# Kernel optimization log

Measured on AMD Instinct MI355X. Metric: run time of the kernel, lower is better.

Reference implementation:

```python
import jax, jax.numpy as jnp
import numpy as np

K = 16          # knn_graph k
FPS_RATIO = 0.5 # fps ratio
BN_EPS = 1e-5


def knn_idx(p, k):
    # p: [B, N, 3] -> neighbor indices [B, N, k] (loop=True: self included)
    n2 = jnp.sum(p * p, axis=-1)                                  # [B, N]
    d = n2[:, :, None] + n2[:, None, :] - 2.0 * jnp.einsum('bnc,bmc->bnm', p, p)
    _, idx = jax.lax.top_k(-d, k)                                 # smallest distances
    return idx


def gather_nbrs(x, idx):
    # x: [B, N, C], idx: [B, N, k] -> [B, N, k, C]
    return jax.vmap(lambda xb, ib: xb[ib])(x, idx)


def bn_silu(y, g, be):
    # training-mode BatchNorm over all rows (flattened) + SiLU, per PyG MLP defaults
    C = y.shape[-1]
    yf = y.reshape(-1, C)
    mu = jnp.mean(yf, axis=0)
    var = jnp.mean((yf - mu) ** 2, axis=0)
    return jax.nn.silu((y - mu) * jax.lax.rsqrt(var + BN_EPS) * g + be)


def fps_idx(p, m):
    # farthest point sampling on one cloud p: [N, 3], deterministic start at 0
    d0 = jnp.sum((p - p[0]) ** 2, axis=-1)
    def step(mind, _):
        i = jnp.argmax(mind)
        di = jnp.sum((p - p[i]) ** 2, axis=-1)
        return jnp.minimum(mind, di), i.astype(jnp.int32)
    _, idxs = jax.lax.scan(step, d0, None, length=m - 1)
    return jnp.concatenate([jnp.zeros((1,), jnp.int32), idxs])


def setup_inputs() -> dict:
    key = jax.random.key(0)
    ks = jax.random.split(key, 4)
    B, N, zdim = 16, 2048, 256
    return {
        'pos': jax.random.normal(ks[0], (B, N, 3), jnp.float32),
        'W1': jax.random.normal(ks[1], (6, 64), jnp.float32) * (1.0 / np.sqrt(6)),
        'b1': jnp.zeros((64,), jnp.float32),
        'g1': jnp.ones((64,), jnp.float32),
        'be1': jnp.zeros((64,), jnp.float32),
        'W2a': jax.random.normal(ks[2], (67, 128), jnp.float32) * (1.0 / np.sqrt(67)),
        'b2a': jnp.zeros((128,), jnp.float32),
        'g2a': jnp.ones((128,), jnp.float32),
        'be2a': jnp.zeros((128,), jnp.float32),
        'W2b': jax.random.normal(ks[3], (128, zdim), jnp.float32) * (1.0 / np.sqrt(128)),
        'b2b': jnp.zeros((zdim,), jnp.float32),
        'g2b': jnp.ones((zdim,), jnp.float32),
        'be2b': jnp.zeros((zdim,), jnp.float32),
    }


def reference(pos, W1, b1, g1, be1, W2a, b2a, g2a, be2a, W2b, b2b, g2b, be2b):
    B, N, _ = pos.shape
    M = int(N * FPS_RATIO)

    # conv1: knn graph on pos, message = MLP([x_j, pos_j - pos_i]), max-aggr
    idx1 = knn_idx(pos, K)                                  # [B, N, K]
    pos_j = gather_nbrs(pos, idx1)                          # [B, N, K, 3]
    msg = jnp.concatenate([pos_j, pos_j - pos[:, :, None, :]], axis=-1)  # [B,N,K,6]
    h = bn_silu(msg @ W1 + b1, g1, be1)                     # [B, N, K, 64]
    h = jnp.max(h, axis=2)                                  # [B, N, 64]

    # farthest point sampling, ratio 0.5
    idx_f = jax.vmap(fps_idx, in_axes=(0, None))(pos, M)    # [B, M]
    h = jax.vmap(lambda a, i: a[i])(h, idx_f)               # [B, M, 64]
    pos2 = jax.vmap(lambda a, i: a[i])(pos, idx_f)          # [B, M, 3]

    # conv2: knn on sampled points, message = MLP2([h_j, pos_j - pos_i]), max-aggr
    idx2 = knn_idx(pos2, K)                                 # [B, M, K]
    h_j = gather_nbrs(h, idx2)                              # [B, M, K, 64]
    p_j = gather_nbrs(pos2, idx2)                           # [B, M, K, 3]
    msg2 = jnp.concatenate([h_j, p_j - pos2[:, :, None, :]], axis=-1)  # [B,M,K,67]
    h2 = bn_silu(msg2 @ W2a + b2a, g2a, be2a)               # [B, M, K, 128]
    h2 = bn_silu(h2 @ W2b + b2b, g2b, be2b)                 # [B, M, K, zdim]
    h2 = jnp.max(h2, axis=2)                                # [B, M, zdim]

    # global max aggregation per cloud
    return jnp.max(h2, axis=1)                              # [B, zdim]
```

## Files before the change

kernel.cpp:

```cpp
#include <hip/hip_runtime.h>
#include <hip/hip_bf16.h>

#define NB 16
#define NN 2048
#define KNNK 16
#define MM 1024
#define RC1 (NB*NN*KNNK)
#define RC2 (NB*MM*KNNK)

typedef unsigned long long u64;
typedef __attribute__((ext_vector_type(8))) short short8;
typedef __attribute__((ext_vector_type(4))) float f32x4;

__device__ __forceinline__ float frn_mul(float a, float b){ return __fmul_rn(a,b); }
__device__ __forceinline__ float frn_add(float a, float b){ return __fadd_rn(a,b); }
__device__ __forceinline__ float frn_sub(float a, float b){ return __fsub_rn(a,b); }
__device__ __forceinline__ float silu_f(float x){ return x / (1.0f + __expf(-x)); }
__device__ __forceinline__ u64 umax64(u64 a, u64 b){ return a > b ? a : b; }

__device__ __forceinline__ unsigned f32_sortable(float f){
  unsigned u = __float_as_uint(f);
  return u ^ ((unsigned)((int)u >> 31) | 0x80000000u);
}
__device__ __forceinline__ unsigned short f2bf(float f){
  unsigned u = __float_as_uint(f);
  return (unsigned short)((u + 0x7FFFu + ((u >> 16) & 1u)) >> 16);
}
__device__ __forceinline__ float bf2f(unsigned short h){
  return __uint_as_float(((unsigned)h) << 16);
}

__device__ __forceinline__ void atomicMaxF(unsigned* addr, float v){
  if (v >= 0.f) atomicMax((int*)addr, (int)__float_as_uint(v));
  else          atomicMin(addr, __float_as_uint(v));
}
__device__ __forceinline__ void atomicMinF(unsigned* addr, float v){
  if (v >= 0.f) atomicMin((int*)addr, (int)__float_as_uint(v));
  else          atomicMax(addr, __float_as_uint(v));
}

__global__ __launch_bounds__(256) void init_kernel(float* stats1, float* stats2a, float* stats2b,
                                                   unsigned* gmax, unsigned* gmin){
  int t = blockIdx.x*256 + threadIdx.x;
  if (t < 128) stats1[t] = 0.f;
  if (t < 256) stats2a[t] = 0.f;
  if (t < 512) stats2b[t] = 0.f;
  if (t < 4096){ gmax[t] = 0xFF800000u; gmin[t] = 0x7F800000u; }
}

template<int CNT>
__device__ __forceinline__ void knn_scan(const float4* pts, int jbase,
                                         float xi, float yi, float zi, float n2i, u64* best){
#pragma unroll
  for (int p = 0; p < KNNK; ++p) best[p] = ~0ull;
  for (int jj = 0; jj < CNT; ++jj){
    float4 v = pts[jbase + jj];
    float e = frn_add(frn_add(frn_mul(xi,v.x), frn_mul(yi,v.y)), frn_mul(zi,v.z));
    float d = frn_sub(frn_add(n2i, v.w), frn_mul(2.0f, e));
    u64 key = ((u64)f32_sortable(d) << 32) | (unsigned)(jbase + jj);
    if (key < best[KNNK-1]){
      u64 cur = key;
#pragma unroll
      for (int p = 0; p < KNNK; ++p){
        u64 mn = best[p] < cur ? best[p] : cur;
        u64 mx = best[p] < cur ? cur : best[p];
        best[p] = mn; cur = mx;
      }
    }
  }
}

__global__ __launch_bounds__(256) void k0_fps_knn1(const float* __restrict__ pos,
    int* __restrict__ idxf, float* __restrict__ pos2, int* __restrict__ idx1,
    const float* __restrict__ W1, const float* __restrict__ b1, float* __restrict__ stats1){
  __shared__ __align__(16) char smem[77*1024];
  int tid = threadIdx.x;
  if (blockIdx.x < 16){
    int b = blockIdx.x;
    float4* pts4 = (float4*)smem;
    int* sel = (int*)(smem + 32*1024);
    u64* wred = (u64*)(smem + 36*1024);
    const float* pb = pos + (size_t)b*NN*3;
    float X[8], Y[8], Z[8], MD[8];
    unsigned LO[8];
#pragma unroll
    for (int q = 0; q < 8; ++q){
      int p = tid + 256*q;
      float x = pb[p*3+0], y = pb[p*3+1], z = pb[p*3+2];
      X[q] = x; Y[q] = y; Z[q] = z;
      LO[q] = ~(unsigned)p;
      pts4[p] = make_float4(x, y, z, 0.f);
    }
    float qx = pb[0], qy = pb[1], qz = pb[2];
#pragma unroll
    for (int q = 0; q < 8; ++q){
      float dx = frn_sub(X[q],qx), dy = frn_sub(Y[q],qy), dz = frn_sub(Z[q],qz);
      MD[q] = frn_add(frn_add(frn_mul(dx,dx), frn_mul(dy,dy)), frn_mul(dz,dz));
    }
    if (tid == 0) sel[0] = 0;
    int wv = tid >> 6;
    __syncthreads();
    for (int s = 1; s < MM; ++s){
      u64 t0 = umax64(((u64)__float_as_uint(MD[0])<<32)|LO[0], ((u64)__float_as_uint(MD[1])<<32)|LO[1]);
      u64 t1 = umax64(((u64)__float_as_uint(MD[2])<<32)|LO[2], ((u64)__float_as_uint(MD[3])<<32)|LO[3]);
      u64 t2 = umax64(((u64)__float_as_uint(MD[4])<<32)|LO[4], ((u64)__float_as_uint(MD[5])<<32)|LO[5]);
      u64 t3 = umax64(((u64)__float_as_uint(MD[6])<<32)|LO[6], ((u64)__float_as_uint(MD[7])<<32)|LO[7]);
      u64 kk = umax64(umax64(t0, t1), umax64(t2, t3));
#define RED_DPP(CTRL) { \
      unsigned lo_ = (unsigned)kk, hi_ = (unsigned)(kk>>32); \
      unsigned plo = (unsigned)__builtin_amdgcn_update_dpp((int)lo_,(int)lo_,CTRL,0xF,0xF,false); \
      unsigned phi = (unsigned)__builtin_amdgcn_update_dpp((int)hi_,(int)hi_,CTRL,0xF,0xF,false); \
      u64 o = ((u64)phi<<32)|plo; kk = o > kk ? o : kk; }
      RED_DPP(0xB1)
      RED_DPP(0x4E)
      RED_DPP(0x124)
      RED_DPP(0x128)
      RED_DPP(0x142)
      RED_DPP(0x143)
#undef RED_DPP
      int par = s & 1;
      if ((tid & 63) == 63) wred[par*4 + wv] = kk;
      __syncthreads();
      const u64* wr = wred + par*4;
      u64 K = umax64(umax64(wr[0], wr[1]), umax64(wr[2], wr[3]));
      unsigned wp = ~(unsigned)K;
      if (tid == 0) sel[s] = (int)wp;
      float4 wc = pts4[wp];
#pragma unroll
      for (int q = 0; q < 8; ++q){
        float dx = frn_sub(X[q],wc.x), dy = frn_sub(Y[q],wc.y), dz = frn_sub(Z[q],wc.z);
        float d = frn_add(frn_add(frn_mul(dx,dx), frn_mul(dy,dy)), frn_mul(dz,dz));
        MD[q] = fminf(MD[q], d);
      }
    }
    __syncthreads();
    for (int m = tid; m < MM; m += 256){
      int j = sel[m];
      idxf[b*MM + m] = j;
      float4 c = pts4[j];
      pos2[(size_t)(b*MM+m)*3+0] = c.x;
      pos2[(size_t)(b*MM+m)*3+1] = c.y;
      pos2[(size_t)(b*MM+m)*3+2] = c.z;
    }
  } else {
    int cid = blockIdx.x - 16;
    int b = cid >> 4;
    int rb16 = cid & 15;
    float4* pts4 = (float4*)smem;
    u64* cres = (u64*)(smem + 32*1024);
    int* idxl = (int*)(smem + 32*1024 + 34816);
    float* red = (float*)(smem + 32*1024 + 34816 + 8704);
    const float* pb = pos + (size_t)b*NN*3;
    for (int i = tid; i < NN; i += 256){
      float x = pb[i*3+0], y = pb[i*3+1], z = pb[i*3+2];
      float n2 = frn_add(frn_add(frn_mul(x,x), frn_mul(y,y)), frn_mul(z,z));
      pts4[i] = make_float4(x, y, z, n2);
    }
    __syncthreads();
    int lrow = tid & 127;
    int ch = tid >> 7;
    int i = rb16*128 + lrow;
    float4 qv = pts4[i];
    u64 best[KNNK];
    knn_scan<1024>(pts4, ch*1024, qv.x, qv.y, qv.z, qv.w, best);
#pragma unroll
    for (int p = 0; p < KNNK; ++p) cres[tid*17 + p] = best[p];
    __syncthreads();
    if (tid < 128){
      const u64* A = cres + tid*17;
      const u64* B = cres + (tid + 128)*17;
      int ia = 0, ib = 0;
      int* op = idx1 + ((size_t)(b*NN + rb16*128 + tid))*KNNK;
#pragma unroll
      for (int p = 0; p < KNNK; ++p){
        u64 ka = A[ia], kb = B[ib];
        int v;
        if (ka < kb){ v = (int)(unsigned)ka; ++ia; }
        else        { v = (int)(unsigned)kb; ++ib; }
        op[p] = v;
        idxl[tid*17 + p] = v;
      }
    }
    __syncthreads();
    int lane = tid & 63, wv = tid >> 6;
    float w[6];
#pragma unroll
    for (int f = 0; f < 6; ++f) w[f] = W1[f*64 + lane];
    float bias = b1[lane];
    float ssum = 0.f, ssq = 0.f;
    for (int r = 0; r < 32; ++r){
      int lr = wv*32 + r;
      float4 pi = pts4[rb16*128 + lr];
      const int* ip = idxl + lr*17;
#pragma unroll 4
      for (int k = 0; k < KNNK; ++k){
        int j = ip[k];
        float4 pj = pts4[j];
        float y = bias;
        y = fmaf(pj.x, w[0], y); y = fmaf(pj.y, w[1], y); y = fmaf(pj.z, w[2], y);
        y = fmaf(pj.x - pi.x, w[3], y); y = fmaf(pj.y - pi.y, w[4], y); y = fmaf(pj.z - pi.z, w[5], y);
        ssum += y; ssq = fmaf(y, y, ssq);
      }
    }
    red[(wv*64+lane)*2+0] = ssum; red[(wv*64+lane)*2+1] = ssq;
    __syncthreads();
    if (tid < 64){
      float s = red[(0*64+lane)*2]+red[(1*64+lane)*2]+red[(2*64+lane)*2]+red[(3*64+lane)*2];
      float q = red[(0*64+lane)*2+1]+red[(1*64+lane)*2+1]+red[(2*64+lane)*2+1]+red[(3*64+lane)*2+1];
      atomicAdd(&stats1[lane], s);
      atomicAdd(&stats1[64+lane], q);
    }
  }
}

__global__ __launch_bounds__(256) void k1_knn2_c1apply(
    const float* __restrict__ pos2, int* __restrict__ idx2,
    const float* __restrict__ pos, const int* __restrict__ idx1,
    const float* __restrict__ W1, const float* __restrict__ b1,
    const float* __restrict__ g1, const float* __restrict__ be1,
    const float* __restrict__ stats1, unsigned short* __restrict__ hbf){
  __shared__ __align__(16) char smem[48*1024];
  int tid = threadIdx.x;
  if (blockIdx.x < 256){
    int b = blockIdx.x >> 4;
    int rb = blockIdx.x & 15;
    float4* sm = (float4*)smem;
    u64* cres = (u64*)(smem + 16*1024);
    const float* pb = pos2 + (size_t)b*MM*3;
    for (int t = tid; t < MM; t += 256){
      float x = pb[t*3+0], y = pb[t*3+1], z = pb[t*3+2];
      float n2 = frn_add(frn_add(frn_mul(x,x), frn_mul(y,y)), frn_mul(z,z));
      sm[t] = make_float4(x, y, z, n2);
    }
    __syncthreads();
    int trow = tid & 63, ch = tid >> 6;
    int i = rb*64 + trow;
    float4 qv = sm[i];
    u64 best[KNNK];
    knn_scan<256>(sm, ch*256, qv.x, qv.y, qv.z, qv.w, best);
#pragma unroll
    for (int p = 0; p < KNNK; ++p) cres[tid*KNNK + p] = best[p];
    __syncthreads();
    if (tid < 64){
      const u64* L0 = cres + tid*KNNK;
      const u64* L1 = cres + (64 + tid)*KNNK;
      const u64* L2 = cres + (128 + tid)*KNNK;
      const u64* L3 = cres + (192 + tid)*KNNK;
      int o0=0, o1=0, o2=0, o3=0;
      int* op = idx2 + ((size_t)(b*MM + rb*64 + tid))*KNNK;
#pragma unroll
      for (int p = 0; p < KNNK; ++p){
        u64 k0 = L0[o0], k1 = L1[o1], k2 = L2[o2], k3 = L3[o3];
        u64 m01 = k0 < k1 ? k0 : k1;
        u64 m23 = k2 < k3 ? k2 : k3;
        u64 m = m01 < m23 ? m01 : m23;
        op[p] = (int)(unsigned)m;
        o0 += (m == k0); o1 += (m == k1); o2 += (m == k2); o3 += (m == k3);
      }
    }
  } else {
    float4* pts4 = (float4*)smem;
    int bblk = blockIdx.x - 256;
    int b = bblk >> 6;
    const float* pb = pos + (size_t)b*NN*3;
    for (int i = tid; i < NN; i += 256)
      pts4[i] = make_float4(pb[i*3+0], pb[i*3+1], pb[i*3+2], 0.f);
    __syncthreads();
    int lane = tid & 63, wv = tid >> 6;
    int wave = bblk*4 + wv;
    float w[6];
#pragma unroll
    for (int f = 0; f < 6; ++f) w[f] = W1[f*64 + lane];
    float bias = b1[lane];
    const float inv = 1.0f / (float)RC1;
    float mu = stats1[lane] * inv;
    float var = fmaxf(stats1[64+lane]*inv - mu*mu, 0.f);
    float sc = rsqrtf(var + 1e-5f) * g1[lane];
    float sh = be1[lane] - mu*sc;
    for (int r = 0; r < 8; ++r){
      int row = wave*8 + r;
      int ii = row & 2047;
      float4 pi = pts4[ii];
      const int* ip = idx1 + (size_t)row * KNNK;
      float ymn = INFINITY, ymx = -INFINITY;
#pragma unroll 4
      for (int k = 0; k < KNNK; ++k){
        int j = ip[k];
        float4 pj = pts4[j];
        float y = bias;
        y = fmaf(pj.x, w[0], y); y = fmaf(pj.y, w[1], y); y = fmaf(pj.z, w[2], y);
        y = fmaf(pj.x - pi.x, w[3], y); y = fmaf(pj.y - pi.y, w[4], y); y = fmaf(pj.z - pi.z, w[5], y);
        ymn = fminf(ymn, y); ymx = fmaxf(ymx, y);
      }
      hbf[((size_t)row << 6) + lane] = f2bf(fmaxf(silu_f(fmaf(ymx, sc, sh)), silu_f(fmaf(ymn, sc, sh))));
    }
  }
}

__global__ __launch_bounds__(256) void conv2a_kernel(
    const unsigned short* __restrict__ hbf, const int* __restrict__ idxf,
    const float* __restrict__ pos2, const int* __restrict__ idx2,
    const float* __restrict__ W2a, const float* __restrict__ b2a,
    float* __restrict__ stats2a, __hip_bfloat16* __restrict__ y2a){
  __shared__ __align__(16) unsigned short At[64*104];
  __shared__ __align__(16) unsigned short Wt[128*104];
  __shared__ int qs[64];
  int tid = threadIdx.x;
  int lane = tid & 63, wvi = tid >> 6;
  for (int i = tid; i < 96*128; i += 256){
    int k = i >> 7, c = i & 127;
    Wt[c*104 + k] = (k < 67) ? f2bf(W2a[k*128 + c]) : (unsigned short)0;
  }
  for (int i = tid; i < 64*104/2; i += 256) ((unsigned*)At)[i] = 0u;
  __syncthreads();
  int cb = wvi*32;
  short8 bfrag[2][3];
#pragma unroll
  for (int cf = 0; cf < 2; ++cf)
#pragma unroll
    for (int kf = 0; kf < 3; ++kf){
      int col = cb + cf*16 + (lane & 15);
      bfrag[cf][kf] = *(short8*)(Wt + col*104 + kf*32 + (lane>>4)*8);
    }
  float bb[2] = { b2a[cb + (lane & 15)], b2a[cb + 16 + (lane & 15)] };
  float ssum[2] = {0.f, 0.f}, ssq[2] = {0.f, 0.f};
  for (int t = 0; t < 4; ++t){
    int tbase = (blockIdx.x*4 + t)*64;
    if (t > 0) __syncthreads();
    if (tid < 64){
      int grow = tbase + tid;
      int b = grow >> 14;
      int m = (grow >> 4) & 1023;
      int j = idx2[grow];
      int q = idxf[b*MM + j];
      qs[tid] = b*NN + q;
      const float* pm = pos2 + ((size_t)(b*MM + m))*3;
      const float* pj = pos2 + ((size_t)(b*MM + j))*3;
      At[tid*104 + 64] = f2bf(pj[0]-pm[0]);
      At[tid*104 + 65] = f2bf(pj[1]-pm[1]);
      At[tid*104 + 66] = f2bf(pj[2]-pm[2]);
    }
    __syncthreads();
    {
      int r = tid & 63, ck = tid >> 6;
      const unsigned short* src = hbf + (size_t)qs[r]*64 + ck*16;
      short8 v0 = *(const short8*)(src);
      short8 v1 = *(const short8*)(src + 8);
      *(short8*)(At + r*104 + ck*16) = v0;
      *(short8*)(At + r*104 + ck*16 + 8) = v1;
    }
    __syncthreads();
#pragma unroll
    for (int rf = 0; rf < 4; ++rf){
      int r = rf*16 + (lane & 15);
      short8 af[3];
#pragma unroll
      for (int kf = 0; kf < 3; ++kf)
        af[kf] = *(short8*)(At + r*104 + kf*32 + (lane>>4)*8);
#pragma unroll
      for (int cf = 0; cf < 2; ++cf){
        f32x4 acc = {0.f,0.f,0.f,0.f};
#pragma unroll
        for (int kf = 0; kf < 3; ++kf)
          acc = __builtin_amdgcn_mfma_f32_16x16x32_bf16(af[kf], bfrag[cf][kf], acc, 0, 0, 0);
#pragma unroll
        for (int jj = 0; jj < 4; ++jj){
          int row = tbase + rf*16 + (lane>>4)*4 + jj;
          int col = cb + cf*16 + (lane & 15);
          float y = acc[jj] + bb[cf];
          ssum[cf] += y; ssq[cf] = fmaf(y, y, ssq[cf]);
          y2a[(size_t)row*128 + col] = __float2bfloat16(y);
        }
      }
    }
  }
#pragma unroll
  for (int cf = 0; cf < 2; ++cf){
#pragma unroll
    for (int off = 16; off <= 32; off += 16){
      ssum[cf] += __shfl_xor(ssum[cf], off);
      ssq[cf]  += __shfl_xor(ssq[cf],  off);
    }
  }
  if ((lane >> 4) == 0){
    atomicAdd(&stats2a[cb + lane], ssum[0]);
    atomicAdd(&stats2a[128 + cb + lane], ssq[0]);
    atomicAdd(&stats2a[cb + 16 + lane], ssum[1]);
    atomicAdd(&stats2a[128 + cb + 16 + lane], ssq[1]);
  }
}

__global__ __launch_bounds__(256) void conv2b_kernel(
    const __hip_bfloat16* __restrict__ y2a, const float* __restrict__ stats2a,
    const float* __restrict__ g2a, const float* __restrict__ be2a,
    const float* __restrict__ W2b, const float* __restrict__ b2b,
    float* __restrict__ stats2b, unsigned* __restrict__ gmax, unsigned* __restrict__ gmin){
  __shared__ __align__(16) char Albs[64*256];
  __shared__ __align__(16) char Btbs[128*256];
  __shared__ float sc2a[128], sh2a[128];
  int tid = threadIdx.x;
  int lane = tid & 63, wvi = tid >> 6;
  int ct = blockIdx.x & 1;
  int rb = blockIdx.x >> 1;
  int c0 = ct * 128;
  int batch = rb >> 5;
  if (tid < 128){
    const float inv = 1.0f / (float)RC2;
    float mu = stats2a[tid] * inv;
    float var = fmaxf(stats2a[128+tid]*inv - mu*mu, 0.f);
    float s = rsqrtf(var + 1e-5f) * g2a[tid];
    sc2a[tid] = s; sh2a[tid] = be2a[tid] - mu*s;
  }
  {
    int cc = tid & 127, u0 = tid >> 7;
#pragma unroll
    for (int i = 0; i < 8; ++i){
      int u = u0 + i*2;
      unsigned short hb[8];
#pragma unroll
      for (int e = 0; e < 8; ++e) hb[e] = f2bf(W2b[(size_t)(u*8+e)*256 + c0 + cc]);
      *(short8*)(Btbs + cc*256 + u*16) = *(short8*)hb;
    }
  }
  __syncthreads();
  short8 bfrag[2][4];
#pragma unroll
  for (int cf = 0; cf < 2; ++cf)
#pragma unroll
    for (int kb4 = 0; kb4 < 4; ++kb4){
      int col_local = wvi*32 + cf*16 + (lane & 15);
      bfrag[cf][kb4] = *(short8*)(Btbs + col_local*256 + kb4*64 + (lane>>4)*16);
    }
  float bb[2] = { b2b[c0 + wvi*32 + (lane & 15)], b2b[c0 + wvi*32 + 16 + (lane & 15)] };
  float vmn[2] = {INFINITY, INFINITY}, vmx[2] = {-INFINITY, -INFINITY};
  float ssum[2] = {0.f, 0.f}, ssq[2] = {0.f, 0.f};
  const unsigned short* y2u = (const unsigned short*)y2a;
  int sr = tid & 63, su = tid >> 6;
  for (int tile = 0; tile < 8; ++tile){
    int row0 = rb*512 + tile*64;
    if (tile > 0) __syncthreads();
#pragma unroll
    for (int i = 0; i < 4; ++i){
      int u = su + i*4;
      short8 v = *(const short8*)(y2u + (size_t)(row0 + sr)*128 + u*8);
      unsigned short ha[8];
#pragma unroll
      for (int e = 0; e < 8; ++e){
        int k = u*8 + e;
        float f = bf2f((unsigned short)v[e]);
        ha[e] = f2bf(silu_f(fmaf(f, sc2a[k], sh2a[k])));
      }
      *(short8*)(Albs + sr*256 + ((u*16) ^ ((sr & 7) << 4))) = *(short8*)ha;
    }
    __syncthreads();
#pragma unroll
    for (int sl = 0; sl < 4; ++sl){
      int r = sl*16 + (lane & 15);
      short8 af[4];
#pragma unroll
      for (int kb4 = 0; kb4 < 4; ++kb4)
        af[kb4] = *(short8*)(Albs + r*256 + ((kb4*64 + (lane>>4)*16) ^ ((r & 7) << 4)));
#pragma unroll
      for (int cf = 0; cf < 2; ++cf){
        f32x4 acc = {0.f, 0.f, 0.f, 0.f};
#pragma unroll
        for (int kb4 = 0; kb4 < 4; ++kb4)
          acc = __builtin_amdgcn_mfma_f32_16x16x32_bf16(af[kb4], bfrag[cf][kb4], acc, 0, 0, 0);
#pragma unroll
        for (int j = 0; j < 4; ++j){
          float y = acc[j] + bb[cf];
          vmn[cf] = fminf(vmn[cf], y); vmx[cf] = fmaxf(vmx[cf], y);
          ssum[cf] += y; ssq[cf] = fmaf(y, y, ssq[cf]);
        }
      }
    }
  }
#pragma unroll
  for (int cf = 0; cf < 2; ++cf){
#pragma unroll
    for (int off = 16; off <= 32; off += 16){
      vmn[cf]  = fminf(vmn[cf],  __shfl_xor(vmn[cf],  off));
      vmx[cf]  = fmaxf(vmx[cf],  __shfl_xor(vmx[cf],  off));
      ssum[cf] = ssum[cf] + __shfl_xor(ssum[cf], off);
      ssq[cf]  = ssq[cf]  + __shfl_xor(ssq[cf],  off);
    }
  }
  if ((lane >> 4) == 0){
#pragma unroll
    for (int cf = 0; cf < 2; ++cf){
      int c = c0 + wvi*32 + cf*16 + lane;
      atomicAdd(&stats2b[c], ssum[cf]);
      atomicAdd(&stats2b[256+c], ssq[cf]);
      atomicMaxF(&gmax[batch*256 + c], vmx[cf]);
      atomicMinF(&gmin[batch*256 + c], vmn[cf]);
    }
  }
}

__global__ __launch_bounds__(256) void final_kernel(
    const float* __restrict__ stats2b, const unsigned* __restrict__ gmax,
    const unsigned* __restrict__ gmin, const float* __restrict__ g2b,
    const float* __restrict__ be2b, float* __restrict__ out){
  int t = blockIdx.x*256 + threadIdx.x;
  if (t >= NB*256) return;
  int c = t & 255;
  const float inv = 1.0f / (float)RC2;
  float mu = stats2b[c]*inv;
  float var = fmaxf(stats2b[256+c]*inv - mu*mu, 0.f);
  float sc = rsqrtf(var + 1e-5f)*g2b[c];
  float sh = be2b[c] - mu*sc;
  float mx = __uint_as_float(gmax[t]);
  float mn = __uint_as_float(gmin[t]);
  out[t] = fmaxf(silu_f(fmaf(mx, sc, sh)), silu_f(fmaf(mn, sc, sh)));
}

extern "C" void kernel_launch(void* const* d_in, const int* in_sizes, int n_in,
                              void* d_out, int out_size, void* d_ws, size_t ws_size,
                              hipStream_t stream){
  (void)in_sizes; (void)n_in; (void)out_size; (void)ws_size;
  const float* pos  = (const float*)d_in[0];
  const float* W1   = (const float*)d_in[1];
  const float* b1   = (const float*)d_in[2];
  const float* g1   = (const float*)d_in[3];
  const float* be1  = (const float*)d_in[4];
  const float* W2a  = (const float*)d_in[5];
  const float* b2a  = (const float*)d_in[6];
  const float* g2a  = (const float*)d_in[7];
  const float* be2a = (const float*)d_in[8];
  const float* W2b  = (const float*)d_in[9];
  const float* b2b  = (const float*)d_in[10];
  const float* g2b  = (const float*)d_in[11];
  const float* be2b = (const float*)d_in[12];

  char* w = (char*)d_ws;
  size_t off = 0;
  auto carve = [&](size_t bytes)->void*{ void* p = w + off; off += (bytes + 255) & ~(size_t)255; return p; };
  int*      idx1    = (int*)carve((size_t)NB*NN*KNNK*4);
  unsigned short* hbf = (unsigned short*)carve((size_t)NB*NN*64*2);
  int*      idxf    = (int*)carve((size_t)NB*MM*4);
  float*    pos2    = (float*)carve((size_t)NB*MM*3*4);
  int*      idx2    = (int*)carve((size_t)NB*MM*KNNK*4);
  float*    stats1  = (float*)carve(128*4);
  float*    stats2a = (float*)carve(256*4);
  float*    stats2b = (float*)carve(512*4);
  unsigned* gmax    = (unsigned*)carve(4096*4);
  unsigned* gmin    = (unsigned*)carve(4096*4);
  __hip_bfloat16* y2a = (__hip_bfloat16*)carve((size_t)RC2*128*2);

  init_kernel<<<dim3(16), dim3(256), 0, stream>>>(stats1, stats2a, stats2b, gmax, gmin);
  k0_fps_knn1<<<dim3(272), dim3(256), 0, stream>>>(pos, idxf, pos2, idx1, W1, b1, stats1);
  k1_knn2_c1apply<<<dim3(1280), dim3(256), 0, stream>>>(pos2, idx2, pos, idx1, W1, b1, g1, be1, stats1, hbf);
  conv2a_kernel<<<dim3(1024), dim3(256), 0, stream>>>(hbf, idxf, pos2, idx2, W2a, b2a, stats2a, y2a);
  conv2b_kernel<<<dim3(1024), dim3(256), 0, stream>>>(y2a, stats2a, g2a, be2a, W2b, b2b, stats2b, gmax, gmin);
  final_kernel<<<dim3(16), dim3(256), 0, stream>>>(stats2b, gmax, gmin, g2b, be2b, (float*)d_out);
}
```

Before: 801.8 us.

## Split FPS across two kernels to overlap with knn1 and conv1 apply

Farthest point sampling is split at step 512. The first half runs alongside the knn1/stats blocks and saves its running min-distance state to global memory. The second half resumes inside the conv1-apply kernel, so the serial FPS chain overlaps with more parallel work. knn2 moves into its own kernel launched afterwards, which adds one launch and a small state round-trip through memory.

```diff
diff --git a/kernel.cpp b/kernel.cpp
--- a/kernel.cpp
+++ b/kernel.cpp
@@ -5,6 +5,7 @@
 #define NN 2048
 #define KNNK 16
 #define MM 1024
+#define FSPLIT 512
 #define RC1 (NB*NN*KNNK)
 #define RC2 (NB*MM*KNNK)
 
@@ -70,9 +71,48 @@
   }
 }
 
-__global__ __launch_bounds__(256) void k0_fps_knn1(const float* __restrict__ pos,
+__device__ __forceinline__ void fps_span(float4* pts4, int* sel, u64* wred,
+    float X[8], float Y[8], float Z[8], float MD[8], const unsigned LO[8],
+    int s0, int s1, int tid, int wv){
+  for (int s = s0; s < s1; ++s){
+    u64 t0 = umax64(((u64)__float_as_uint(MD[0])<<32)|LO[0], ((u64)__float_as_uint(MD[1])<<32)|LO[1]);
+    u64 t1 = umax64(((u64)__float_as_uint(MD[2])<<32)|LO[2], ((u64)__float_as_uint(MD[3])<<32)|LO[3]);
+    u64 t2 = umax64(((u64)__float_as_uint(MD[4])<<32)|LO[4], ((u64)__float_as_uint(MD[5])<<32)|LO[5]);
+    u64 t3 = umax64(((u64)__float_as_uint(MD[6])<<32)|LO[6], ((u64)__float_as_uint(MD[7])<<32)|LO[7]);
+    u64 kk = umax64(umax64(t0, t1), umax64(t2, t3));
+#define RED_DPP(CTRL) { \
+    unsigned lo_ = (unsigned)kk, hi_ = (unsigned)(kk>>32); \
+    unsigned plo = (unsigned)__builtin_amdgcn_update_dpp((int)lo_,(int)lo_,CTRL,0xF,0xF,false); \
+    unsigned phi = (unsigned)__builtin_amdgcn_update_dpp((int)hi_,(int)hi_,CTRL,0xF,0xF,false); \
+    u64 o = ((u64)phi<<32)|plo; kk = o > kk ? o : kk; }
+    RED_DPP(0xB1)
+    RED_DPP(0x4E)
+    RED_DPP(0x124)
+    RED_DPP(0x128)
+    RED_DPP(0x142)
+    RED_DPP(0x143)
+#undef RED_DPP
+    int par = s & 1;
+    if ((tid & 63) == 63) wred[par*4 + wv] = kk;
+    __syncthreads();
+    const u64* wr = wred + par*4;
+    u64 K = umax64(umax64(wr[0], wr[1]), umax64(wr[2], wr[3]));
+    unsigned wp = ~(unsigned)K;
+    if (tid == 0) sel[s] = (int)wp;
+    float4 wc = pts4[wp];
+#pragma unroll
+    for (int q = 0; q < 8; ++q){
+      float dx = frn_sub(X[q],wc.x), dy = frn_sub(Y[q],wc.y), dz = frn_sub(Z[q],wc.z);
+      float d = frn_add(frn_add(frn_mul(dx,dx), frn_mul(dy,dy)), frn_mul(dz,dz));
+      MD[q] = fminf(MD[q], d);
+    }
+  }
+}
+
+__global__ __launch_bounds__(256) void kA(const float* __restrict__ pos,
     int* __restrict__ idxf, float* __restrict__ pos2, int* __restrict__ idx1,
-    const float* __restrict__ W1, const float* __restrict__ b1, float* __restrict__ stats1){
+    const float* __restrict__ W1, const float* __restrict__ b1, float* __restrict__ stats1,
+    float* __restrict__ mdsave){
   __shared__ __align__(16) char smem[77*1024];
   int tid = threadIdx.x;
   if (blockIdx.x < 16){
@@ -100,41 +140,9 @@
     if (tid == 0) sel[0] = 0;
     int wv = tid >> 6;
     __syncthreads();
-    for (int s = 1; s < MM; ++s){
-      u64 t0 = umax64(((u64)__float_as_uint(MD[0])<<32)|LO[0], ((u64)__float_as_uint(MD[1])<<32)|LO[1]);
-      u64 t1 = umax64(((u64)__float_as_uint(MD[2])<<32)|LO[2], ((u64)__float_as_uint(MD[3])<<32)|LO[3]);
-      u64 t2 = umax64(((u64)__float_as_uint(MD[4])<<32)|LO[4], ((u64)__float_as_uint(MD[5])<<32)|LO[5]);
-      u64 t3 = umax64(((u64)__float_as_uint(MD[6])<<32)|LO[6], ((u64)__float_as_uint(MD[7])<<32)|LO[7]);
-      u64 kk = umax64(umax64(t0, t1), umax64(t2, t3));
-#define RED_DPP(CTRL) { \
-      unsigned lo_ = (unsigned)kk, hi_ = (unsigned)(kk>>32); \
-      unsigned plo = (unsigned)__builtin_amdgcn_update_dpp((int)lo_,(int)lo_,CTRL,0xF,0xF,false); \
-      unsigned phi = (unsigned)__builtin_amdgcn_update_dpp((int)hi_,(int)hi_,CTRL,0xF,0xF,false); \
-      u64 o = ((u64)phi<<32)|plo; kk = o > kk ? o : kk; }
-      RED_DPP(0xB1)
-      RED_DPP(0x4E)
-      RED_DPP(0x124)
-      RED_DPP(0x128)
-      RED_DPP(0x142)
-      RED_DPP(0x143)
-#undef RED_DPP
-      int par = s & 1;
-      if ((tid & 63) == 63) wred[par*4 + wv] = kk;
-      __syncthreads();
-      const u64* wr = wred + par*4;
-      u64 K = umax64(umax64(wr[0], wr[1]), umax64(wr[2], wr[3]));
-      unsigned wp = ~(unsigned)K;
-      if (tid == 0) sel[s] = (int)wp;
-      float4 wc = pts4[wp];
-#pragma unroll
-      for (int q = 0; q < 8; ++q){
-        float dx = frn_sub(X[q],wc.x), dy = frn_sub(Y[q],wc.y), dz = frn_sub(Z[q],wc.z);
-        float d = frn_add(frn_add(frn_mul(dx,dx), frn_mul(dy,dy)), frn_mul(dz,dz));
-        MD[q] = fminf(MD[q], d);
-      }
-    }
-    __syncthreads();
-    for (int m = tid; m < MM; m += 256){
+    fps_span(pts4, sel, wred, X, Y, Z, MD, LO, 1, FSPLIT, tid, wv);
+    __syncthreads();
+    for (int m = tid; m < FSPLIT; m += 256){
       int j = sel[m];
       idxf[b*MM + m] = j;
       float4 c = pts4[j];
@@ -142,6 +150,8 @@
       pos2[(size_t)(b*MM+m)*3+1] = c.y;
       pos2[(size_t)(b*MM+m)*3+2] = c.z;
     }
+#pragma unroll
+    for (int q = 0; q < 8; ++q) mdsave[b*NN + tid + 256*q] = MD[q];
   } else {
     int cid = blockIdx.x - 16;
     int b = cid >> 4;
@@ -213,54 +223,46 @@
   }
 }
 
-__global__ __launch_bounds__(256) void k1_knn2_c1apply(
-    const float* __restrict__ pos2, int* __restrict__ idx2,
-    const float* __restrict__ pos, const int* __restrict__ idx1,
+__global__ __launch_bounds__(256) void kB(const float* __restrict__ pos,
+    int* __restrict__ idxf, float* __restrict__ pos2, const int* __restrict__ idx1,
     const float* __restrict__ W1, const float* __restrict__ b1,
     const float* __restrict__ g1, const float* __restrict__ be1,
-    const float* __restrict__ stats1, unsigned short* __restrict__ hbf){
-  __shared__ __align__(16) char smem[48*1024];
+    const float* __restrict__ stats1, unsigned short* __restrict__ hbf,
+    const float* __restrict__ mdsave){
+  __shared__ __align__(16) char smem[41*1024];
   int tid = threadIdx.x;
-  if (blockIdx.x < 256){
-    int b = blockIdx.x >> 4;
-    int rb = blockIdx.x & 15;
-    float4* sm = (float4*)smem;
-    u64* cres = (u64*)(smem + 16*1024);
-    const float* pb = pos2 + (size_t)b*MM*3;
-    for (int t = tid; t < MM; t += 256){
-      float x = pb[t*3+0], y = pb[t*3+1], z = pb[t*3+2];
-      float n2 = frn_add(frn_add(frn_mul(x,x), frn_mul(y,y)), frn_mul(z,z));
-      sm[t] = make_float4(x, y, z, n2);
-    }
-    __syncthreads();
-    int trow = tid & 63, ch = tid >> 6;
-    int i = rb*64 + trow;
-    float4 qv = sm[i];
-    u64 best[KNNK];
-    knn_scan<256>(sm, ch*256, qv.x, qv.y, qv.z, qv.w, best);
-#pragma unroll
-    for (int p = 0; p < KNNK; ++p) cres[tid*KNNK + p] = best[p];
-    __syncthreads();
-    if (tid < 64){
-      const u64* L0 = cres + tid*KNNK;
-      const u64* L1 = cres + (64 + tid)*KNNK;
-      const u64* L2 = cres + (128 + tid)*KNNK;
-      const u64* L3 = cres + (192 + tid)*KNNK;
-      int o0=0, o1=0, o2=0, o3=0;
-      int* op = idx2 + ((size_t)(b*MM + rb*64 + tid))*KNNK;
-#pragma unroll
-      for (int p = 0; p < KNNK; ++p){
-        u64 k0 = L0[o0], k1 = L1[o1], k2 = L2[o2], k3 = L3[o3];
-        u64 m01 = k0 < k1 ? k0 : k1;
-        u64 m23 = k2 < k3 ? k2 : k3;
-        u64 m = m01 < m23 ? m01 : m23;
-        op[p] = (int)(unsigned)m;
-        o0 += (m == k0); o1 += (m == k1); o2 += (m == k2); o3 += (m == k3);
-      }
+  if (blockIdx.x < 16){
+    int b = blockIdx.x;
+    float4* pts4 = (float4*)smem;
+    int* sel = (int*)(smem + 32*1024);
+    u64* wred = (u64*)(smem + 36*1024);
+    const float* pb = pos + (size_t)b*NN*3;
+    float X[8], Y[8], Z[8], MD[8];
+    unsigned LO[8];
+#pragma unroll
+    for (int q = 0; q < 8; ++q){
+      int p = tid + 256*q;
+      float x = pb[p*3+0], y = pb[p*3+1], z = pb[p*3+2];
+      X[q] = x; Y[q] = y; Z[q] = z;
+      LO[q] = ~(unsigned)p;
+      pts4[p] = make_float4(x, y, z, 0.f);
+      MD[q] = mdsave[b*NN + p];
+    }
+    int wv = tid >> 6;
+    __syncthreads();
+    fps_span(pts4, sel, wred, X, Y, Z, MD, LO, FSPLIT, MM, tid, wv);
+    __syncthreads();
+    for (int m = FSPLIT + tid; m < MM; m += 256){
+      int j = sel[m];
+      idxf[b*MM + m] = j;
+      float4 c = pts4[j];
+      pos2[(size_t)(b*MM+m)*3+0] = c.x;
+      pos2[(size_t)(b*MM+m)*3+1] = c.y;
+      pos2[(size_t)(b*MM+m)*3+2] = c.z;
     }
   } else {
     float4* pts4 = (float4*)smem;
-    int bblk = blockIdx.x - 256;
+    int bblk = blockIdx.x - 16;
     int b = bblk >> 6;
     const float* pb = pos + (size_t)b*NN*3;
     for (int i = tid; i < NN; i += 256)
@@ -297,6 +299,48 @@
   }
 }
 
+__global__ __launch_bounds__(256) void k1_knn2(
+    const float* __restrict__ pos2, int* __restrict__ idx2){
+  __shared__ __align__(16) char smem[48*1024];
+  int tid = threadIdx.x;
+  int b = blockIdx.x >> 4;
+  int rb = blockIdx.x & 15;
+  float4* sm = (float4*)smem;
+  u64* cres = (u64*)(smem + 16*1024);
+  const float* pb = pos2 + (size_t)b*MM*3;
+  for (int t = tid; t < MM; t += 256){
+    float x = pb[t*3+0], y = pb[t*3+1], z = pb[t*3+2];
+    float n2 = frn_add(frn_add(frn_mul(x,x), frn_mul(y,y)), frn_mul(z,z));
+    sm[t] = make_float4(x, y, z, n2);
+  }
+  __syncthreads();
+  int trow = tid & 63, ch = tid >> 6;
+  int i = rb*64 + trow;
+  float4 qv = sm[i];
+  u64 best[KNNK];
+  knn_scan<256>(sm, ch*256, qv.x, qv.y, qv.z, qv.w, best);
+#pragma unroll
+  for (int p = 0; p < KNNK; ++p) cres[tid*KNNK + p] = best[p];
+  __syncthreads();
+  if (tid < 64){
+    const u64* L0 = cres + tid*KNNK;
+    const u64* L1 = cres + (64 + tid)*KNNK;
+    const u64* L2 = cres + (128 + tid)*KNNK;
+    const u64* L3 = cres + (192 + tid)*KNNK;
+    int o0=0, o1=0, o2=0, o3=0;
+    int* op = idx2 + ((size_t)(b*MM + rb*64 + tid))*KNNK;
+#pragma unroll
+    for (int p = 0; p < KNNK; ++p){
+      u64 k0 = L0[o0], k1 = L1[o1], k2 = L2[o2], k3 = L3[o3];
+      u64 m01 = k0 < k1 ? k0 : k1;
+      u64 m23 = k2 < k3 ? k2 : k3;
+      u64 m = m01 < m23 ? m01 : m23;
+      op[p] = (int)(unsigned)m;
+      o0 += (m == k0); o1 += (m == k1); o2 += (m == k2); o3 += (m == k3);
+    }
+  }
+}
+
 __global__ __launch_bounds__(256) void conv2a_kernel(
     const unsigned short* __restrict__ hbf, const int* __restrict__ idxf,
     const float* __restrict__ pos2, const int* __restrict__ idx2,
@@ -545,11 +589,13 @@
   float*    stats2b = (float*)carve(512*4);
   unsigned* gmax    = (unsigned*)carve(4096*4);
   unsigned* gmin    = (unsigned*)carve(4096*4);
+  float*    mdsave  = (float*)carve((size_t)NB*NN*4);
   __hip_bfloat16* y2a = (__hip_bfloat16*)carve((size_t)RC2*128*2);
 
   init_kernel<<<dim3(16), dim3(256), 0, stream>>>(stats1, stats2a, stats2b, gmax, gmin);
-  k0_fps_knn1<<<dim3(272), dim3(256), 0, stream>>>(pos, idxf, pos2, idx1, W1, b1, stats1);
-  k1_knn2_c1apply<<<dim3(1280), dim3(256), 0, stream>>>(pos2, idx2, pos, idx1, W1, b1, g1, be1, stats1, hbf);
+  kA<<<dim3(272), dim3(256), 0, stream>>>(pos, idxf, pos2, idx1, W1, b1, stats1, mdsave);
+  kB<<<dim3(1040), dim3(256), 0, stream>>>(pos, idxf, pos2, idx1, W1, b1, g1, be1, stats1, hbf, mdsave);
+  k1_knn2<<<dim3(256), dim3(256), 0, stream>>>(pos2, idx2);
   conv2a_kernel<<<dim3(1024), dim3(256), 0, stream>>>(hbf, idxf, pos2, idx2, W2a, b2a, stats2a, y2a);
   conv2b_kernel<<<dim3(1024), dim3(256), 0, stream>>>(y2a, stats2a, g2a, be2a, W2b, b2b, stats2b, gmax, gmin);
   final_kernel<<<dim3(16), dim3(256), 0, stream>>>(stats2b, gmax, gmin, g2b, be2b, (float*)d_out);
```

New measurement: 1.018 ms. 27.0% more time.
